# Optimization experiments

Measured on AMD Instinct MI355X. Metric: run time of the kernel, lower is better.

Reference implementation:

```python
import jax, jax.numpy as jnp
import numpy as np

B, T, D = 64, 512, 1024  # batch, step_dim, feature_dim


def setup_inputs() -> dict:
    key = jax.random.key(0)
    k1, k2, k3, k4, k5 = jax.random.split(key, 5)
    x = jax.random.normal(k1, (B, T, D), dtype=jnp.float32)
    mask = jax.random.randint(k2, (B, T), 0, 2).astype(bool)
    mask = mask.at[:, 0].set(True)  # guarantee >=1 valid token per row
    # xavier_uniform bounds
    w_bound = float(np.sqrt(6.0 / (D + D)))
    c_bound = float(np.sqrt(6.0 / (T + 1)))
    weight = jax.random.uniform(k3, (D, D), minval=-w_bound, maxval=w_bound, dtype=jnp.float32)
    context_vector = jax.random.uniform(k4, (T, 1), minval=-c_bound, maxval=c_bound, dtype=jnp.float32)
    b = jnp.zeros((T,), dtype=jnp.float32)
    return {"x": x, "mask": mask, "weight": weight, "context_vector": context_vector, "b": b}


def reference(x, mask, weight, context_vector, b):
    # batched bilinear scores: eij[b,t,s] = x[b,t,:] @ W @ x[b,s,:]^T
    xw = jnp.einsum('btd,de->bte', x, weight)          # [B,T,D]
    eij = jnp.einsum('bte,bse->bts', xw, x)            # [B,T,T]
    # bias over last axis (matches view(-1, T) + b), tanh
    eij = jnp.tanh(eij + b)                            # [B,T,T]
    # context-vector reduction over last axis -> [B,T]
    scores = jnp.einsum('bts,s->bt', eij, context_vector[:, 0])
    # masked softmax over T
    scores = jnp.where(mask, scores, -jnp.inf)
    a = jax.nn.softmax(scores, axis=1)                 # [B,T]
    # weighted sum of inputs -> [B,D]
    out = jnp.einsum('btd,bt->bd', x, a)
    return (out, a)
```

## Files before the change

### kernel.cpp

```cpp
#include <hip/hip_runtime.h>
#include <hip/hip_bf16.h>
#include <math.h>

#define B_ 64
#define T_ 512
#define D_ 1024
#define M_ (B_*T_)

typedef unsigned short u16;
typedef __attribute__((ext_vector_type(8))) _Float16 f16x8;
typedef __attribute__((ext_vector_type(4))) float f32x4;

__device__ __forceinline__ u16 f2h(float f) {
  union { _Float16 h; u16 u; } v;
  v.h = (_Float16)f;
  return v.u;
}

__device__ __forceinline__ float h2f(u16 u) {
  union { u16 u; _Float16 h; } v;
  v.u = u;
  return (float)v.h;
}

__device__ __forceinline__ float fast_tanh(float x) {
  return 1.0f - 2.0f / (__expf(2.0f * x) + 1.0f);
}

__device__ __forceinline__ void gll16(const void* g, void* l) {
  __builtin_amdgcn_global_load_lds(
      (const __attribute__((address_space(1))) unsigned int*)g,
      (__attribute__((address_space(3))) unsigned int*)l, 16, 0, 0);
}

__global__ __launch_bounds__(256) void cvt_kernel(const float4* __restrict__ x,
                                                  ushort4* __restrict__ xh,
                                                  const float* __restrict__ W,
                                                  u16* __restrict__ wt) {
  __shared__ float tile[32][33];
  const int bid = blockIdx.x;
  if (bid < 32768) {
    int i = bid * 256 + threadIdx.x;
    float4 v = x[i];
    ushort4 o;
    o.x = f2h(v.x); o.y = f2h(v.y); o.z = f2h(v.z); o.w = f2h(v.w);
    xh[i] = o;
  } else {
    const int tb = bid - 32768;
    const int n0 = (tb & 31) * 32, k0 = (tb >> 5) * 32;
    const int tx = threadIdx.x & 31, ty = threadIdx.x >> 5;
#pragma unroll
    for (int ph = 0; ph < 4; ph++)
      tile[ty + ph * 8][tx] = W[(k0 + ty + ph * 8) * D_ + n0 + tx];
    __syncthreads();
#pragma unroll
    for (int ph = 0; ph < 4; ph++)
      wt[(long)(n0 + ty + ph * 8) * D_ + k0 + tx] = f2h(tile[tx][ty + ph * 8]);
  }
}

struct Stage {
  const u16* gA[2]; const u16* gB[2];
  u16* lA[2]; u16* lB[2];
  int t;
  __device__ __forceinline__ void issue() {
    const int sb = (t & 3) * 8192;
#pragma unroll
    for (int j = 0; j < 2; j++) {
      gll16(gA[j], lA[j] + sb);
      gll16(gB[j], lB[j] + sb);
      gA[j] += 32; gB[j] += 32;
    }
    t++;
  }
};

template<int VMN>
__device__ __forceinline__ void core_step(Stage& st, bool do_issue,
                                          const u16* ra, const u16* rb, int buf,
                                          f32x4 (&acc)[8][4]) {
  if constexpr (VMN == 8)      asm volatile("s_waitcnt vmcnt(8)" ::: "memory");
  else if constexpr (VMN == 4) asm volatile("s_waitcnt vmcnt(4)" ::: "memory");
  else                         asm volatile("s_waitcnt vmcnt(0)" ::: "memory");
  __builtin_amdgcn_s_barrier();
  asm volatile("" ::: "memory");
  __builtin_amdgcn_sched_barrier(0);
  if (do_issue) st.issue();
  const u16* rat = ra + buf * 8192;
  const u16* rbt = rb + buf * 8192;
  f16x8 af[8], bfr[4];
#pragma unroll
  for (int i = 0; i < 8; i++) af[i] = *(const f16x8*)(rat + i * 512);
#pragma unroll
  for (int i = 0; i < 4; i++) bfr[i] = *(const f16x8*)(rbt + i * 512);
  __builtin_amdgcn_s_setprio(1);
#pragma unroll
  for (int mi = 0; mi < 8; mi++)
#pragma unroll
    for (int ni = 0; ni < 4; ni++)
      acc[mi][ni] = __builtin_amdgcn_mfma_f32_16x16x32_f16(af[mi], bfr[ni], acc[mi][ni], 0, 0, 0);
  __builtin_amdgcn_s_setprio(0);
}

__device__ __forceinline__ void gemm_core256(const u16* __restrict__ Abase,
                                             const u16* __restrict__ Bbase,
                                             u16* As, u16* Bs, int tid,
                                             f32x4 (&acc)[8][4]) {
  const int wave = tid >> 6, lane = tid & 63;
  const int swz_c = ((lane & 3) - ((lane >> 3) & 3)) & 3;
  const int rin = lane >> 2;
  Stage st; st.t = 0;
#pragma unroll
  for (int j = 0; j < 2; j++) {
    const int ci = wave * 2 + j;
    st.gA[j] = Abase + (long)(ci * 16 + rin) * D_ + swz_c * 8;
    st.lA[j] = As + ci * 512;
    st.gB[j] = Bbase + (long)(ci * 16 + rin) * D_ + swz_c * 8;
    st.lB[j] = Bs + ci * 512;
  }
  st.issue(); st.issue(); st.issue();
  const int wrow = (wave >> 2) * 128, wcol = (wave & 3) * 64;
  const int lm = lane & 15, qd = lane >> 4;
  const int swz_r = ((qd + (lm >> 1)) & 3) * 8;
  const u16* ra = As + (wrow + lm) * 32 + swz_r;
  const u16* rb = Bs + (wcol + lm) * 32 + swz_r;
#pragma unroll 1
  for (int t = 0; t < 30; t++)
    core_step<8>(st, t < 29, ra, rb, t & 3, acc);
  core_step<4>(st, false, ra, rb, 30 & 3, acc);
  core_step<0>(st, false, ra, rb, 31 & 3, acc);
}

__global__ __launch_bounds__(512, 2) void gemm1_kernel(const u16* __restrict__ xh,
                                                       const u16* __restrict__ wt,
                                                       u16* __restrict__ xw) {
  __shared__ u16 As[4 * 8192];
  __shared__ u16 Bs[4 * 8192];
  f32x4 acc[8][4] = {};
  const int tid = threadIdx.x;
  const int bx = blockIdx.x;
  const int xcd = bx & 7, j = bx >> 3;
  const int mt = xcd * 16 + (j >> 2);
  const int nt = j & 3;
  const long m0 = (long)mt * 256, n0 = (long)nt * 256;
  gemm_core256(xh + m0 * D_, wt + n0 * D_, As, Bs, tid, acc);

  const int wave = tid >> 6, lane = tid & 63;
  const int wrow = (wave >> 2) * 128, wcol = (wave & 3) * 64;
  const int lm = lane & 15, qd = lane >> 4;
#pragma unroll
  for (int mi = 0; mi < 8; mi++)
#pragma unroll
    for (int ni = 0; ni < 4; ni++) {
      long m = m0 + wrow + mi * 16 + qd * 4;
      long n = n0 + wcol + ni * 16 + lm;
      u16* ptr = xw + m * D_ + n;
#pragma unroll
      for (int r = 0; r < 4; r++) ptr[(long)r * D_] = f2h(acc[mi][ni][r]);
    }
}

__global__ __launch_bounds__(512, 2) void gemm2_kernel(const u16* __restrict__ xw,
                                                       const u16* __restrict__ xh,
                                                       const float* __restrict__ bias,
                                                       const float* __restrict__ cv,
                                                       float* __restrict__ scores_part) {
  __shared__ u16 As[4 * 8192];
  __shared__ u16 Bs[4 * 8192];
  f32x4 acc[8][4] = {};
  const int tid = threadIdx.x;
  const int bx = blockIdx.x;
  const int xcd = bx & 7, j = bx >> 3;
  const int bb = xcd * 8 + (j >> 2);
  const int tile = j & 3;
  const int tt = tile >> 1, st_ = tile & 1;
  const long arow = (long)bb * T_ + tt * 256;
  const long brow = (long)bb * T_ + st_ * 256;
  gemm_core256(xw + arow * D_, xh + brow * D_, As, Bs, tid, acc);

  const int wave = tid >> 6, lane = tid & 63;
  const int wrow = (wave >> 2) * 128, wcol = (wave & 3) * 64;
  const int lm = lane & 15, qd = lane >> 4;
  float cvv[4], bv[4];
#pragma unroll
  for (int ni = 0; ni < 4; ni++) {
    int s = st_ * 256 + wcol + ni * 16 + lm;
    cvv[ni] = cv[s];
    bv[ni] = bias[s];
  }
  const int plane = st_ * 4 + (wave & 3);
  float* dst = scores_part + plane * (B_ * T_) + bb * T_ + tt * 256;
#pragma unroll
  for (int mi = 0; mi < 8; mi++) {
#pragma unroll
    for (int r = 0; r < 4; r++) {
      float p = 0.f;
#pragma unroll
      for (int ni = 0; ni < 4; ni++) p += fast_tanh(acc[mi][ni][r] + bv[ni]) * cvv[ni];
      p += __shfl_xor(p, 1); p += __shfl_xor(p, 2);
      p += __shfl_xor(p, 4); p += __shfl_xor(p, 8);
      if (lm == 0) dst[wrow + mi * 16 + qd * 4 + r] = p;
    }
  }
}

__global__ __launch_bounds__(256) void sm_wsum_kernel(const float* __restrict__ sp,
                                                      const unsigned char* __restrict__ m8,
                                                      const u16* __restrict__ xh,
                                                      float* __restrict__ a_out,
                                                      float* __restrict__ out) {
  __shared__ float a_sh[512];
  __shared__ float red[8];
  __shared__ int nonz;
  __shared__ float4 lred[4][64];
  const int b = blockIdx.x, dq = blockIdx.y, tid = threadIdx.x;
  const int w = tid >> 6, ln = tid & 63;
  if (tid == 0) nonz = 0;
  __syncthreads();
  {
    unsigned char c = m8[tid * 4 + 1] | m8[tid * 4 + 2] | m8[tid * 4 + 3] |
                      m8[(tid + 256) * 4 + 1] | m8[(tid + 256) * 4 + 2] | m8[(tid + 256) * 4 + 3];
    if (c) atomicOr(&nonz, 1);
  }
  __syncthreads();
  const bool is_i32 = (nonz == 0);
  float v[2]; bool valid[2];
#pragma unroll
  for (int h = 0; h < 2; h++) {
    int t = tid + h * 256;
    int idx = b * T_ + t;
    valid[h] = is_i32 ? (m8[(long)idx * 4] != 0) : (m8[idx] != 0);
    float s = 0.f;
#pragma unroll
    for (int pl = 0; pl < 8; pl++) s += sp[pl * (B_ * T_) + idx];
    v[h] = valid[h] ? s : -INFINITY;
  }
  float m = fmaxf(v[0], v[1]);
#pragma unroll
  for (int o = 32; o > 0; o >>= 1) m = fmaxf(m, __shfl_xor(m, o));
  if (ln == 0) red[w] = m;
  __syncthreads();
  const float rowmax = fmaxf(fmaxf(red[0], red[1]), fmaxf(red[2], red[3]));
  float e0 = valid[0] ? expf(v[0] - rowmax) : 0.f;
  float e1 = valid[1] ? expf(v[1] - rowmax) : 0.f;
  float ss = e0 + e1;
#pragma unroll
  for (int o = 32; o > 0; o >>= 1) ss += __shfl_xor(ss, o);
  if (ln == 0) red[4 + w] = ss;
  __syncthreads();
  const float tot = red[4] + red[5] + red[6] + red[7];
  const float a0 = e0 / tot, a1 = e1 / tot;
  a_sh[tid] = a0; a_sh[tid + 256] = a1;
  if (dq == 0) {
    a_out[b * T_ + tid] = a0;
    a_out[b * T_ + tid + 256] = a1;
  }
  __syncthreads();
  const int d0 = dq * 256 + ln * 4;
  const u16* xp = xh + (long)b * T_ * D_ + d0;
  float4 acc = make_float4(0.f, 0.f, 0.f, 0.f);
  for (int i = 0; i < 128; i++) {
    int t = w * 128 + i;
    float av = a_sh[t];
    ushort4 xv = *(const ushort4*)(xp + (long)t * D_);
    acc.x += av * h2f(xv.x); acc.y += av * h2f(xv.y);
    acc.z += av * h2f(xv.z); acc.w += av * h2f(xv.w);
  }
  lred[w][ln] = acc;
  __syncthreads();
  if (w == 0) {
    float4 s0 = lred[0][ln], s1 = lred[1][ln], s2 = lred[2][ln], s3 = lred[3][ln];
    float4 s;
    s.x = s0.x + s1.x + s2.x + s3.x;
    s.y = s0.y + s1.y + s2.y + s3.y;
    s.z = s0.z + s1.z + s2.z + s3.z;
    s.w = s0.w + s1.w + s2.w + s3.w;
    *(float4*)(out + (long)b * D_ + d0) = s;
  }
}

extern "C" void kernel_launch(void* const* d_in, const int* in_sizes, int n_in,
                              void* d_out, int out_size, void* d_ws, size_t ws_size,
                              hipStream_t stream) {
  const float* x = (const float*)d_in[0];
  const unsigned char* mask = (const unsigned char*)d_in[1];
  const float* W = (const float*)d_in[2];
  const float* cv = (const float*)d_in[3];
  const float* bias = (const float*)d_in[4];

  float* out = (float*)d_out;
  float* a_out = out + (size_t)B_ * D_;

  char* ws = (char*)d_ws;
  u16* xh = (u16*)(ws);
  u16* wt = (u16*)(ws + 67108864);
  float* scores_part = (float*)(ws + 67108864);
  u16* xw = (u16*)(ws + 69206016);

  cvt_kernel<<<32768 + 1024, 256, 0, stream>>>((const float4*)x, (ushort4*)xh, W, wt);
  gemm1_kernel<<<512, 512, 0, stream>>>(xh, wt, xw);
  gemm2_kernel<<<256, 512, 0, stream>>>(xw, xh, bias, cv, scores_part);
  sm_wsum_kernel<<<dim3(B_, 4), 256, 0, stream>>>(scores_part, mask, xh, a_out, out);
}
```

Measured before the change: 342.2 us.

## Split GEMM k-step into two MFMA halves interleaved with LDS reads and loads

Restructures the main GEMM loop so each k-step runs in two halves. The A fragments and half the B fragments are read from LDS, A global-to-LDS loads are issued, and MFMAs run for two output columns. The other B fragments and B loads are interleaved before the second MFMA half. The loop is also unrolled by the 4 LDS ring slots so buffer offsets become compile-time constants. The goal is to overlap LDS reads and global issue with MFMA work, at the cost of extra barriers per step and a more fragile wait-count schedule.

```diff
diff --git a/kernel.cpp b/kernel.cpp
--- a/kernel.cpp
+++ b/kernel.cpp
@@ -63,43 +63,62 @@
   const u16* gA[2]; const u16* gB[2];
   u16* lA[2]; u16* lB[2];
   int t;
-  __device__ __forceinline__ void issue() {
+  __device__ __forceinline__ void issueA() {
     const int sb = (t & 3) * 8192;
-#pragma unroll
-    for (int j = 0; j < 2; j++) {
-      gll16(gA[j], lA[j] + sb);
-      gll16(gB[j], lB[j] + sb);
-      gA[j] += 32; gB[j] += 32;
-    }
+    gll16(gA[0], lA[0] + sb); gA[0] += 32;
+    gll16(gA[1], lA[1] + sb); gA[1] += 32;
+  }
+  __device__ __forceinline__ void issueB() {
+    const int sb = (t & 3) * 8192;
+    gll16(gB[0], lB[0] + sb); gB[0] += 32;
+    gll16(gB[1], lB[1] + sb); gB[1] += 32;
     t++;
   }
 };
 
-template<int VMN>
-__device__ __forceinline__ void core_step(Stage& st, bool do_issue,
-                                          const u16* ra, const u16* rb, int buf,
-                                          f32x4 (&acc)[8][4]) {
+__device__ __forceinline__ void mfma_acc(f32x4& a, f16x8 x, f16x8 y) {
+  a = __builtin_amdgcn_mfma_f32_16x16x32_f16(x, y, a, 0, 0, 0);
+}
+
+template<int SLOT, int VMN, bool ISSUE>
+__device__ __forceinline__ void step256(Stage& st, const u16* ra, const u16* rb,
+                                        f32x4 (&acc)[8][4]) {
+  const u16* rat = ra + SLOT * 8192;
+  const u16* rbt = rb + SLOT * 8192;
+  f16x8 af[8], bf0, bf1;
+#pragma unroll
+  for (int i = 0; i < 8; i++) af[i] = *(const f16x8*)(rat + i * 512);
+  bf0 = *(const f16x8*)(rbt);
+  bf1 = *(const f16x8*)(rbt + 512);
+  if (ISSUE) st.issueA();
+  __builtin_amdgcn_s_barrier();
+  asm volatile("s_waitcnt lgkmcnt(0)" ::: "memory");
+  __builtin_amdgcn_sched_barrier(0);
+  __builtin_amdgcn_s_setprio(1);
+#pragma unroll
+  for (int mi = 0; mi < 8; mi++) {
+    mfma_acc(acc[mi][0], af[mi], bf0);
+    mfma_acc(acc[mi][1], af[mi], bf1);
+  }
+  __builtin_amdgcn_s_setprio(0);
+  __builtin_amdgcn_s_barrier();
+  f16x8 bf2 = *(const f16x8*)(rbt + 2 * 512);
+  f16x8 bf3 = *(const f16x8*)(rbt + 3 * 512);
+  if (ISSUE) st.issueB();
   if constexpr (VMN == 8)      asm volatile("s_waitcnt vmcnt(8)" ::: "memory");
   else if constexpr (VMN == 4) asm volatile("s_waitcnt vmcnt(4)" ::: "memory");
-  else                         asm volatile("s_waitcnt vmcnt(0)" ::: "memory");
-  __builtin_amdgcn_s_barrier();
-  asm volatile("" ::: "memory");
+  else if constexpr (VMN == 0) asm volatile("s_waitcnt vmcnt(0)" ::: "memory");
+  __builtin_amdgcn_s_barrier();
+  asm volatile("s_waitcnt lgkmcnt(0)" ::: "memory");
   __builtin_amdgcn_sched_barrier(0);
-  if (do_issue) st.issue();
-  const u16* rat = ra + buf * 8192;
-  const u16* rbt = rb + buf * 8192;
-  f16x8 af[8], bfr[4];
-#pragma unroll
-  for (int i = 0; i < 8; i++) af[i] = *(const f16x8*)(rat + i * 512);
-#pragma unroll
-  for (int i = 0; i < 4; i++) bfr[i] = *(const f16x8*)(rbt + i * 512);
   __builtin_amdgcn_s_setprio(1);
 #pragma unroll
-  for (int mi = 0; mi < 8; mi++)
-#pragma unroll
-    for (int ni = 0; ni < 4; ni++)
-      acc[mi][ni] = __builtin_amdgcn_mfma_f32_16x16x32_f16(af[mi], bfr[ni], acc[mi][ni], 0, 0, 0);
+  for (int mi = 0; mi < 8; mi++) {
+    mfma_acc(acc[mi][2], af[mi], bf2);
+    mfma_acc(acc[mi][3], af[mi], bf3);
+  }
   __builtin_amdgcn_s_setprio(0);
+  __builtin_amdgcn_s_barrier();
 }
 
 __device__ __forceinline__ void gemm_core256(const u16* __restrict__ Abase,
@@ -118,17 +137,29 @@
     st.gB[j] = Bbase + (long)(ci * 16 + rin) * D_ + swz_c * 8;
     st.lB[j] = Bs + ci * 512;
   }
-  st.issue(); st.issue(); st.issue();
+  st.issueA(); st.issueB();
+  st.issueA(); st.issueB();
+  st.issueA(); st.issueB();
+  asm volatile("s_waitcnt vmcnt(8)" ::: "memory");
+  __builtin_amdgcn_s_barrier();
+
   const int wrow = (wave >> 2) * 128, wcol = (wave & 3) * 64;
   const int lm = lane & 15, qd = lane >> 4;
   const int swz_r = ((qd + (lm >> 1)) & 3) * 8;
   const u16* ra = As + (wrow + lm) * 32 + swz_r;
   const u16* rb = Bs + (wcol + lm) * 32 + swz_r;
+
 #pragma unroll 1
-  for (int t = 0; t < 30; t++)
-    core_step<8>(st, t < 29, ra, rb, t & 3, acc);
-  core_step<4>(st, false, ra, rb, 30 & 3, acc);
-  core_step<0>(st, false, ra, rb, 31 & 3, acc);
+  for (int it = 0; it < 7; ++it) {
+    step256<0, 8, true>(st, ra, rb, acc);
+    step256<1, 8, true>(st, ra, rb, acc);
+    step256<2, 8, true>(st, ra, rb, acc);
+    step256<3, 8, true>(st, ra, rb, acc);
+  }
+  step256<0, 8, true >(st, ra, rb, acc);
+  step256<1, 4, false>(st, ra, rb, acc);
+  step256<2, 0, false>(st, ra, rb, acc);
+  step256<3, -1, false>(st, ra, rb, acc);
 }
 
 __global__ __launch_bounds__(512, 2) void gemm1_kernel(const u16* __restrict__ xh,
```

Measured after the change: 327.3 us. -4.4%, faster.
